# Kernel optimization log

Hardware: AMD Instinct MI355X
Metric: run time of the kernel (lower is better)

The kernel has to match this reference:

```python
import jax, jax.numpy as jnp
import numpy as np

H = 8        # num_heads
D = 768      # d_model
DH = D // H  # d_head = 96


def setup_inputs() -> dict:
    key = jax.random.key(0)
    ks = jax.random.split(key, 12)
    B, S = 4, 2048
    s_in = 1.0 / np.sqrt(D)
    s_cat = 1.0 / np.sqrt(D)
    return {
        "input_querys": jax.random.normal(ks[0], (B, S, D), jnp.float32),
        "input_key": jax.random.normal(ks[1], (B, S, D), jnp.float32),
        "input_values": jax.random.normal(ks[2], (B, S, D), jnp.float32),
        # per-head projection weights, stacked over the head axis
        "Wq": jax.random.normal(ks[3], (H, D, DH), jnp.float32) * s_in,
        "bq": jax.random.normal(ks[4], (H, DH), jnp.float32) * s_in,
        "Wk": jax.random.normal(ks[5], (H, D, DH), jnp.float32) * s_in,
        "bk": jax.random.normal(ks[6], (H, DH), jnp.float32) * s_in,
        "Wv": jax.random.normal(ks[7], (H, D, DH), jnp.float32) * s_in,
        "bv": jax.random.normal(ks[8], (H, DH), jnp.float32) * s_in,
        # output linear: (H*DH) -> D
        "Wo": jax.random.normal(ks[9], (H * DH, D), jnp.float32) * s_cat,
        "bo": jax.random.normal(ks[10], (D,), jnp.float32) * s_cat,
    }


def reference(input_querys, input_key, input_values, Wq, bq, Wk, bk, Wv, bv, Wo, bo):
    # Per-head linear projections (vectorized over the head axis)
    # q/k/v: [B,S,D] -> [B,H,S,DH]
    Q = jnp.einsum("bsd,hdk->bhsk", input_querys, Wq) + bq[None, :, None, :]
    K = jnp.einsum("bsd,hdk->bhsk", input_key, Wk) + bk[None, :, None, :]
    V = jnp.einsum("bsd,hdk->bhsk", input_values, Wv) + bv[None, :, None, :]

    scale = 1.0 / jnp.sqrt(jnp.asarray(DH, Q.dtype))
    scores = jnp.einsum("bhsk,bhtk->bhst", Q, K) * scale  # [B,H,S,S]
    attn = jax.nn.softmax(scores, axis=-1)
    out = jnp.einsum("bhst,bhtk->bhsk", attn, V)  # [B,H,S,DH]

    # concat heads (head-major order matches torch.cat over ModuleList)
    B, _, S, _ = out.shape
    cat = out.transpose(0, 2, 1, 3).reshape(B, S, H * DH)
    return cat @ Wo + bo
```

## Files before the change

kernel.cpp:

```cpp
#include <hip/hip_runtime.h>


typedef unsigned short u16;
typedef _Float16 h16;
typedef h16 h16x8 __attribute__((ext_vector_type(8)));
typedef __fp16 fp16x2 __attribute__((ext_vector_type(2)));
typedef unsigned short u16x8 __attribute__((ext_vector_type(8)));
typedef unsigned short u16x4 __attribute__((ext_vector_type(4)));
typedef float f32x4 __attribute__((ext_vector_type(4)));

__device__ __forceinline__ u16 f2h(float f) {
  union { h16 h; u16 u; } c; c.h = (h16)f; return c.u;
}

__device__ __forceinline__ void gll16(const void* g, void* l) {
  __builtin_amdgcn_global_load_lds(
      (const __attribute__((address_space(1))) void*)g,
      (__attribute__((address_space(3))) void*)l, 16, 0, 0);
}

__global__ __launch_bounds__(256) void prep_kernel(
    const float* __restrict__ Wq, const float* __restrict__ Wk,
    const float* __restrict__ Wv, const float* __restrict__ Wo,
    u16* __restrict__ WqT, u16* __restrict__ WkT,
    u16* __restrict__ WvT, u16* __restrict__ WoT)
{
  int idx = (blockIdx.x * 256 + threadIdx.x) * 8;
  int region = idx / 589824;
  int i = idx % 589824;
  int n = i / 768;
  int d = i % 768;
  u16x8 v;
  if (region == 3) {
    #pragma unroll
    for (int j = 0; j < 8; j++) v[j] = f2h(Wo[(size_t)(d + j) * 768 + n]);
    *(u16x8*)(&WoT[i]) = v;
  } else {
    int h = n / 96, kk = n % 96;
    const float* W = (region == 0) ? Wq : (region == 1) ? Wk : Wv;
    u16* T = (region == 0) ? WqT : (region == 1) ? WkT : WvT;
    #pragma unroll
    for (int j = 0; j < 8; j++) v[j] = f2h(W[(size_t)h * 73728 + (size_t)(d + j) * 96 + kk]);
    *(u16x8*)(&T[i]) = v;
  }
}

#define GK 768

__global__ __launch_bounds__(256) void gemm_qkv(
    const float* __restrict__ Xq, const float* __restrict__ Xk,
    const float* __restrict__ Xv, const u16* __restrict__ WT,
    const float* __restrict__ bq, const float* __restrict__ bk,
    const float* __restrict__ bv,
    u16* __restrict__ Q16, u16* __restrict__ K16, u16* __restrict__ VT)
{
  const int z = blockIdx.z;
  const float* A = (z == 0) ? Xq : (z == 1) ? Xk : Xv;
  const u16* BT = WT + (size_t)z * 589824;
  const float* bias = (z == 0) ? bq : (z == 1) ? bk : bv;

  __shared__ __align__(16) u16 As[128 * 32];
  __shared__ __align__(16) u16 Bs[64 * 32];
  const int tid = threadIdx.x;
  const int wave = tid >> 6;
  const int lane = tid & 63;
  const int quad = lane >> 4;
  const int l16 = lane & 15;
  const int m0 = blockIdx.x * 128;
  const int n0 = blockIdx.y * 64;

  f32x4 acc[2][4];
  #pragma unroll
  for (int i = 0; i < 2; i++)
    #pragma unroll
    for (int j = 0; j < 4; j++) acc[i][j] = (f32x4){0.f, 0.f, 0.f, 0.f};

  const int ar = tid >> 2;
  const int ac = (tid & 3) * 8;

  f32x4 pf[4];
  u16x8 pb;
  {
    pf[0] = *(const f32x4*)(&A[(size_t)(m0 + ar) * GK + ac]);
    pf[1] = *(const f32x4*)(&A[(size_t)(m0 + ar) * GK + ac + 4]);
    pf[2] = *(const f32x4*)(&A[(size_t)(m0 + 64 + ar) * GK + ac]);
    pf[3] = *(const f32x4*)(&A[(size_t)(m0 + 64 + ar) * GK + ac + 4]);
    pb = *(const u16x8*)(&BT[(size_t)(n0 + ar) * GK + ac]);
  }

  for (int kt = 0; kt < 24; kt++) {
    u16x8 h0, h1;
    #pragma unroll
    for (int j = 0; j < 4; j++) {
      h0[j] = f2h(pf[0][j]); h0[4 + j] = f2h(pf[1][j]);
      h1[j] = f2h(pf[2][j]); h1[4 + j] = f2h(pf[3][j]);
    }
    *(u16x8*)(&As[ar * 32 + ac]) = h0;
    *(u16x8*)(&As[(64 + ar) * 32 + ac]) = h1;
    *(u16x8*)(&Bs[ar * 32 + ac]) = pb;
    __syncthreads();

    if (kt + 1 < 24) {
      const int k0 = (kt + 1) * 32;
      pf[0] = *(const f32x4*)(&A[(size_t)(m0 + ar) * GK + k0 + ac]);
      pf[1] = *(const f32x4*)(&A[(size_t)(m0 + ar) * GK + k0 + ac + 4]);
      pf[2] = *(const f32x4*)(&A[(size_t)(m0 + 64 + ar) * GK + k0 + ac]);
      pf[3] = *(const f32x4*)(&A[(size_t)(m0 + 64 + ar) * GK + k0 + ac + 4]);
      pb = *(const u16x8*)(&BT[(size_t)(n0 + ar) * GK + k0 + ac]);
    }

    h16x8 af[2], bf[4];
    #pragma unroll
    for (int mf = 0; mf < 2; mf++)
      af[mf] = *(const h16x8*)(&As[(wave * 32 + mf * 16 + l16) * 32 + quad * 8]);
    #pragma unroll
    for (int nf = 0; nf < 4; nf++)
      bf[nf] = *(const h16x8*)(&Bs[(nf * 16 + l16) * 32 + quad * 8]);
    #pragma unroll
    for (int mf = 0; mf < 2; mf++)
      #pragma unroll
      for (int nf = 0; nf < 4; nf++)
        acc[mf][nf] = __builtin_amdgcn_mfma_f32_16x16x32_f16(af[mf], bf[nf], acc[mf][nf], 0, 0, 0);

    if (kt + 1 < 24) __syncthreads();
  }

  u16* Yr = (z == 0) ? Q16 : K16;
  #pragma unroll
  for (int nf = 0; nf < 4; nf++) {
    const int n = n0 + nf * 16 + l16;
    const float bv2 = bias[n];
    #pragma unroll
    for (int mf = 0; mf < 2; mf++) {
      const int m = m0 + wave * 32 + mf * 16 + quad * 4;
      if (z == 2) {
        const int b = m >> 11, s = m & 2047;
        u16x4 pk;
        #pragma unroll
        for (int r = 0; r < 4; r++) pk[r] = f2h(acc[mf][nf][r] + bv2);
        *(u16x4*)(&VT[(size_t)b * 768 * 2048 + (size_t)n * 2048 + s]) = pk;
      } else {
        #pragma unroll
        for (int r = 0; r < 4; r++)
          Yr[(size_t)(m + r) * GK + n] = f2h(acc[mf][nf][r] + bv2);
      }
    }
  }
}

__global__ __launch_bounds__(256) void gemm_o(
    const u16* __restrict__ A, const u16* __restrict__ BT,
    const float* __restrict__ bias, float* __restrict__ Y)
{
  __shared__ __align__(16) u16 As[128 * 32];
  __shared__ __align__(16) u16 Bs[64 * 32];
  const int tid = threadIdx.x;
  const int wave = tid >> 6;
  const int lane = tid & 63;
  const int quad = lane >> 4;
  const int l16 = lane & 15;
  const int m0 = blockIdx.x * 128;
  const int n0 = blockIdx.y * 64;

  f32x4 acc[2][4];
  #pragma unroll
  for (int i = 0; i < 2; i++)
    #pragma unroll
    for (int j = 0; j < 4; j++) acc[i][j] = (f32x4){0.f, 0.f, 0.f, 0.f};

  const int Lr = lane >> 2, Lc = (lane & 3) * 8;
  const u16* gA0 = A + (size_t)(m0 + wave * 32 + Lr) * GK + Lc;
  const u16* gA1 = gA0 + (size_t)16 * GK;
  const u16* gB  = BT + (size_t)(n0 + wave * 16 + Lr) * GK + Lc;
  u16* lA0 = &As[(wave * 32) * 32];
  u16* lA1 = &As[(wave * 32 + 16) * 32];
  u16* lB  = &Bs[(wave * 16) * 32];

  for (int kt = 0; kt < 24; kt++) {
    gll16(gA0, lA0);
    gll16(gA1, lA1);
    gll16(gB, lB);
    gA0 += 32; gA1 += 32; gB += 32;
    __syncthreads();

    h16x8 af[2], bf[4];
    #pragma unroll
    for (int mf = 0; mf < 2; mf++)
      af[mf] = *(const h16x8*)(&As[(wave * 32 + mf * 16 + l16) * 32 + quad * 8]);
    #pragma unroll
    for (int nf = 0; nf < 4; nf++)
      bf[nf] = *(const h16x8*)(&Bs[(nf * 16 + l16) * 32 + quad * 8]);
    #pragma unroll
    for (int mf = 0; mf < 2; mf++)
      #pragma unroll
      for (int nf = 0; nf < 4; nf++)
        acc[mf][nf] = __builtin_amdgcn_mfma_f32_16x16x32_f16(af[mf], bf[nf], acc[mf][nf], 0, 0, 0);
    __syncthreads();
  }

  #pragma unroll
  for (int nf = 0; nf < 4; nf++) {
    const int n = n0 + nf * 16 + l16;
    const float bv = bias[n];
    #pragma unroll
    for (int mf = 0; mf < 2; mf++) {
      const int m = m0 + wave * 32 + mf * 16 + quad * 4;
      #pragma unroll
      for (int r = 0; r < 4; r++)
        Y[(size_t)(m + r) * GK + n] = acc[mf][nf][r] + bv;
    }
  }
}

#define SEQ 2048
#define LQK 104
#define LVT 72
#define LPS 72

__global__ __launch_bounds__(512, 4) void attn_kernel(
    const u16* __restrict__ Q, const u16* __restrict__ K,
    const u16* __restrict__ VT, u16* __restrict__ O)
{
  __shared__ __align__(16) u16 Ks[64 * LQK];
  __shared__ __align__(16) u16 Vt[96 * LVT];
  __shared__ __align__(16) u16 Ps[8][16 * LPS];

  const int tid = threadIdx.x;
  const int wave = tid >> 6;
  const int lane = tid & 63;
  const int quad = lane >> 4;
  const int l16 = lane & 15;

  const int bh = blockIdx.y;
  const int b = bh >> 3, h = bh & 7;
  const int q0 = blockIdx.x * 128;

  const size_t batch_off = (size_t)b * SEQ * 768;
  const u16* Kg = K + batch_off + h * 96;
  const u16* Vg = VT + (size_t)b * 768 * 2048 + (size_t)(h * 96) * 2048;

  h16x8 qf[3];
  {
    const u16* Qrow = Q + batch_off + (size_t)(q0 + wave * 16 + l16) * 768 + h * 96 + quad * 8;
    #pragma unroll
    for (int ks = 0; ks < 3; ks++) qf[ks] = *(const h16x8*)(&Qrow[ks * 32]);
  }

  const int kr0 = tid / 12, kc0 = (tid % 12) * 8;
  const int kr1 = (tid + 512) / 12, kc1 = ((tid + 512) % 12) * 8;
  const int vr0 = tid >> 3, vc0 = (tid & 7) * 8;
  const int vr1 = (tid + 512) >> 3, vc1 = ((tid + 512) & 7) * 8;
  const bool extra = tid < 256;

  f32x4 o[6];
  #pragma unroll
  for (int i = 0; i < 6; i++) o[i] = (f32x4){0.f, 0.f, 0.f, 0.f};
  float m_raw = -1e30f, lrow = 0.f;
  const float sc = 0.14724498f;

  u16* Pw = &Ps[wave][0];

  u16x8 kA, kB, vA, vB;
  kA = *(const u16x8*)(&Kg[(size_t)kr0 * 768 + kc0]);
  vA = *(const u16x8*)(&Vg[(size_t)vr0 * 2048 + vc0]);
  if (extra) {
    kB = *(const u16x8*)(&Kg[(size_t)kr1 * 768 + kc1]);
    vB = *(const u16x8*)(&Vg[(size_t)vr1 * 2048 + vc1]);
  }

  for (int kt = 0; kt < SEQ / 64; kt++) {
    *(u16x8*)(&Ks[kr0 * LQK + kc0]) = kA;
    *(u16x8*)(&Vt[vr0 * LVT + vc0]) = vA;
    if (extra) {
      *(u16x8*)(&Ks[kr1 * LQK + kc1]) = kB;
      *(u16x8*)(&Vt[vr1 * LVT + vc1]) = vB;
    }
    __syncthreads();

    if (kt + 1 < SEQ / 64) {
      const u16* Kn = Kg + (size_t)(kt + 1) * 64 * 768;
      const u16* Vn = Vg + (size_t)(kt + 1) * 64;
      kA = *(const u16x8*)(&Kn[(size_t)kr0 * 768 + kc0]);
      vA = *(const u16x8*)(&Vn[(size_t)vr0 * 2048 + vc0]);
      if (extra) {
        kB = *(const u16x8*)(&Kn[(size_t)kr1 * 768 + kc1]);
        vB = *(const u16x8*)(&Vn[(size_t)vr1 * 2048 + vc1]);
      }
    }

    f32x4 s[4];
    #pragma unroll
    for (int kf = 0; kf < 4; kf++) s[kf] = (f32x4){0.f, 0.f, 0.f, 0.f};
    #pragma unroll
    for (int ks = 0; ks < 3; ks++) {
      #pragma unroll
      for (int kf = 0; kf < 4; kf++) {
        h16x8 a = *(const h16x8*)(&Ks[(kf * 16 + l16) * LQK + ks * 32 + quad * 8]);
        s[kf] = __builtin_amdgcn_mfma_f32_16x16x32_f16(a, qf[ks], s[kf], 0, 0, 0);
      }
    }

    float mx = s[0][0];
    #pragma unroll
    for (int kf = 0; kf < 4; kf++)
      #pragma unroll
      for (int r = 0; r < 4; r++) mx = fmaxf(mx, s[kf][r]);
    mx = fmaxf(mx, __shfl_xor(mx, 16));
    mx = fmaxf(mx, __shfl_xor(mx, 32));
    const float mold = m_raw;
    m_raw = fmaxf(mold, mx);
    const float c0 = sc * m_raw;
    float ps = 0.f;
    #pragma unroll
    for (int kf = 0; kf < 4; kf++)
      #pragma unroll
      for (int r = 0; r < 4; r++) {
        float p = exp2f(fmaf(s[kf][r], sc, -c0));
        s[kf][r] = p;
        ps += p;
      }
    if (__any(m_raw > mold)) {
      const float alpha = exp2f(sc * (mold - m_raw));
      lrow *= alpha;
      #pragma unroll
      for (int nfo = 0; nfo < 6; nfo++)
        #pragma unroll
        for (int r = 0; r < 4; r++) o[nfo][r] *= alpha;
    }
    lrow += ps;

    #pragma unroll
    for (int kf = 0; kf < 4; kf++)
      #pragma unroll
      for (int rp = 0; rp < 4; rp += 2) {
        fp16x2 pk = __builtin_amdgcn_cvt_pkrtz(s[kf][rp], s[kf][rp + 1]);
        *(fp16x2*)(&Pw[l16 * LPS + kf * 16 + quad * 4 + rp]) = pk;
      }

    #pragma unroll
    for (int ks = 0; ks < 2; ks++) {
      h16x8 pfr = *(const h16x8*)(&Pw[l16 * LPS + ks * 32 + quad * 8]);
      #pragma unroll
      for (int nfo = 0; nfo < 6; nfo++) {
        h16x8 vfr = *(const h16x8*)(&Vt[(nfo * 16 + l16) * LVT + ks * 32 + quad * 8]);
        o[nfo] = __builtin_amdgcn_mfma_f32_16x16x32_f16(vfr, pfr, o[nfo], 0, 0, 0);
      }
    }
    __syncthreads();
  }

  lrow += __shfl_xor(lrow, 16);
  lrow += __shfl_xor(lrow, 32);
  const float inv = 1.0f / lrow;
  u16* Ob = O + batch_off + (size_t)(q0 + wave * 16 + l16) * 768 + h * 96;
  #pragma unroll
  for (int nfo = 0; nfo < 6; nfo++) {
    fp16x2 lo = __builtin_amdgcn_cvt_pkrtz(o[nfo][0] * inv, o[nfo][1] * inv);
    fp16x2 hi = __builtin_amdgcn_cvt_pkrtz(o[nfo][2] * inv, o[nfo][3] * inv);
    *(fp16x2*)(&Ob[nfo * 16 + quad * 4]) = lo;
    *(fp16x2*)(&Ob[nfo * 16 + quad * 4 + 2]) = hi;
  }
}

extern "C" void kernel_launch(void* const* d_in, const int* in_sizes, int n_in,
                              void* d_out, int out_size, void* d_ws, size_t ws_size,
                              hipStream_t stream) {
  const float* Xq = (const float*)d_in[0];
  const float* Xk = (const float*)d_in[1];
  const float* Xv = (const float*)d_in[2];
  const float* Wq = (const float*)d_in[3];
  const float* bq = (const float*)d_in[4];
  const float* Wk = (const float*)d_in[5];
  const float* bk = (const float*)d_in[6];
  const float* Wv = (const float*)d_in[7];
  const float* bv = (const float*)d_in[8];
  const float* Wo = (const float*)d_in[9];
  const float* bo = (const float*)d_in[10];

  u16* wsu = (u16*)d_ws;
  u16* WT  = wsu;
  u16* WoT = wsu + 3 * 589824;
  u16* Q16 = wsu + 4 * 589824;

  u16* outu = (u16*)d_out;
  u16* VTb = outu;
  u16* K16 = outu + 6291456;

  u16* A16 = (u16*)d_in[0];

  prep_kernel<<<1152, 256, 0, stream>>>(Wq, Wk, Wv, Wo, WT, WT + 589824, WT + 2 * 589824, WoT);
  gemm_qkv<<<dim3(64, 12, 3), 256, 0, stream>>>(Xq, Xk, Xv, WT, bq, bk, bv, Q16, K16, VTb);
  attn_kernel<<<dim3(16, 32), 512, 0, stream>>>(Q16, K16, VTb, A16);
  gemm_o<<<dim3(64, 12), 256, 0, stream>>>(A16, WoT, bo, (float*)d_out);
}
```

Baseline: 312.0 us.

## Give each attention wave two query tiles and swap GEMM grid axes

The attention kernel now runs 256-thread blocks where each wave handles 32 query rows as two 16-row sets. Each K and V fragment read from LDS then feeds two MFMAs, which halves LDS fragment traffic per unit of compute. Per-thread register use roughly doubles for accumulators and Q fragments, and launch bounds drop to 256 threads with 3 blocks per SM. Separately, both GEMM launches swap grid x/y so consecutive blocks walk along N and share the same A rows, which should improve cache locality.

After: 355.9 us. +14.1%, slower.

```diff
diff --git a/kernel.cpp b/kernel.cpp
--- a/kernel.cpp
+++ b/kernel.cpp
@@ -66,8 +66,8 @@
   const int lane = tid & 63;
   const int quad = lane >> 4;
   const int l16 = lane & 15;
-  const int m0 = blockIdx.x * 128;
-  const int n0 = blockIdx.y * 64;
+  const int m0 = blockIdx.y * 128;
+  const int n0 = blockIdx.x * 64;
 
   f32x4 acc[2][4];
   #pragma unroll
@@ -159,8 +159,8 @@
   const int lane = tid & 63;
   const int quad = lane >> 4;
   const int l16 = lane & 15;
-  const int m0 = blockIdx.x * 128;
-  const int n0 = blockIdx.y * 64;
+  const int m0 = blockIdx.y * 128;
+  const int n0 = blockIdx.x * 64;
 
   f32x4 acc[2][4];
   #pragma unroll
@@ -217,13 +217,13 @@
 #define LVT 72
 #define LPS 72
 
-__global__ __launch_bounds__(512, 4) void attn_kernel(
+__global__ __launch_bounds__(256, 3) void attn_kernel(
     const u16* __restrict__ Q, const u16* __restrict__ K,
     const u16* __restrict__ VT, u16* __restrict__ O)
 {
   __shared__ __align__(16) u16 Ks[64 * LQK];
   __shared__ __align__(16) u16 Vt[96 * LVT];
-  __shared__ __align__(16) u16 Ps[8][16 * LPS];
+  __shared__ __align__(16) u16 Ps[4][32 * LPS];
 
   const int tid = threadIdx.x;
   const int wave = tid >> 6;
@@ -239,126 +239,140 @@
   const u16* Kg = K + batch_off + h * 96;
   const u16* Vg = VT + (size_t)b * 768 * 2048 + (size_t)(h * 96) * 2048;
 
-  h16x8 qf[3];
-  {
-    const u16* Qrow = Q + batch_off + (size_t)(q0 + wave * 16 + l16) * 768 + h * 96 + quad * 8;
-    #pragma unroll
-    for (int ks = 0; ks < 3; ks++) qf[ks] = *(const h16x8*)(&Qrow[ks * 32]);
-  }
-
-  const int kr0 = tid / 12, kc0 = (tid % 12) * 8;
-  const int kr1 = (tid + 512) / 12, kc1 = ((tid + 512) % 12) * 8;
-  const int vr0 = tid >> 3, vc0 = (tid & 7) * 8;
-  const int vr1 = (tid + 512) >> 3, vc1 = ((tid + 512) & 7) * 8;
-  const bool extra = tid < 256;
-
-  f32x4 o[6];
-  #pragma unroll
-  for (int i = 0; i < 6; i++) o[i] = (f32x4){0.f, 0.f, 0.f, 0.f};
-  float m_raw = -1e30f, lrow = 0.f;
+  h16x8 qf[2][3];
+  #pragma unroll
+  for (int set = 0; set < 2; set++) {
+    const u16* Qrow = Q + batch_off + (size_t)(q0 + wave * 32 + set * 16 + l16) * 768 + h * 96 + quad * 8;
+    #pragma unroll
+    for (int ks = 0; ks < 3; ks++) qf[set][ks] = *(const h16x8*)(&Qrow[ks * 32]);
+  }
+
+  int krr[3], kcc[3], vrr[3], vcc[3];
+  #pragma unroll
+  for (int j = 0; j < 3; j++) {
+    int c = tid + j * 256;
+    krr[j] = c / 12;  kcc[j] = (c % 12) * 8;
+    vrr[j] = c >> 3;  vcc[j] = (c & 7) * 8;
+  }
+
+  f32x4 o[2][6];
+  #pragma unroll
+  for (int set = 0; set < 2; set++)
+    #pragma unroll
+    for (int i = 0; i < 6; i++) o[set][i] = (f32x4){0.f, 0.f, 0.f, 0.f};
+  float m_raw[2] = {-1e30f, -1e30f}, lrow[2] = {0.f, 0.f};
   const float sc = 0.14724498f;
 
   u16* Pw = &Ps[wave][0];
 
-  u16x8 kA, kB, vA, vB;
-  kA = *(const u16x8*)(&Kg[(size_t)kr0 * 768 + kc0]);
-  vA = *(const u16x8*)(&Vg[(size_t)vr0 * 2048 + vc0]);
-  if (extra) {
-    kB = *(const u16x8*)(&Kg[(size_t)kr1 * 768 + kc1]);
-    vB = *(const u16x8*)(&Vg[(size_t)vr1 * 2048 + vc1]);
+  u16x8 kA[3], vA[3];
+  #pragma unroll
+  for (int j = 0; j < 3; j++) {
+    kA[j] = *(const u16x8*)(&Kg[(size_t)krr[j] * 768 + kcc[j]]);
+    vA[j] = *(const u16x8*)(&Vg[(size_t)vrr[j] * 2048 + vcc[j]]);
   }
 
   for (int kt = 0; kt < SEQ / 64; kt++) {
-    *(u16x8*)(&Ks[kr0 * LQK + kc0]) = kA;
-    *(u16x8*)(&Vt[vr0 * LVT + vc0]) = vA;
-    if (extra) {
-      *(u16x8*)(&Ks[kr1 * LQK + kc1]) = kB;
-      *(u16x8*)(&Vt[vr1 * LVT + vc1]) = vB;
+    #pragma unroll
+    for (int j = 0; j < 3; j++) {
+      *(u16x8*)(&Ks[krr[j] * LQK + kcc[j]]) = kA[j];
+      *(u16x8*)(&Vt[vrr[j] * LVT + vcc[j]]) = vA[j];
     }
     __syncthreads();
 
     if (kt + 1 < SEQ / 64) {
       const u16* Kn = Kg + (size_t)(kt + 1) * 64 * 768;
       const u16* Vn = Vg + (size_t)(kt + 1) * 64;
-      kA = *(const u16x8*)(&Kn[(size_t)kr0 * 768 + kc0]);
-      vA = *(const u16x8*)(&Vn[(size_t)vr0 * 2048 + vc0]);
-      if (extra) {
-        kB = *(const u16x8*)(&Kn[(size_t)kr1 * 768 + kc1]);
-        vB = *(const u16x8*)(&Vn[(size_t)vr1 * 2048 + vc1]);
+      #pragma unroll
+      for (int j = 0; j < 3; j++) {
+        kA[j] = *(const u16x8*)(&Kn[(size_t)krr[j] * 768 + kcc[j]]);
+        vA[j] = *(const u16x8*)(&Vn[(size_t)vrr[j] * 2048 + vcc[j]]);
       }
     }
 
-    f32x4 s[4];
-    #pragma unroll
-    for (int kf = 0; kf < 4; kf++) s[kf] = (f32x4){0.f, 0.f, 0.f, 0.f};
+    f32x4 s[2][4];
+    #pragma unroll
+    for (int set = 0; set < 2; set++)
+      #pragma unroll
+      for (int kf = 0; kf < 4; kf++) s[set][kf] = (f32x4){0.f, 0.f, 0.f, 0.f};
     #pragma unroll
     for (int ks = 0; ks < 3; ks++) {
       #pragma unroll
       for (int kf = 0; kf < 4; kf++) {
         h16x8 a = *(const h16x8*)(&Ks[(kf * 16 + l16) * LQK + ks * 32 + quad * 8]);
-        s[kf] = __builtin_amdgcn_mfma_f32_16x16x32_f16(a, qf[ks], s[kf], 0, 0, 0);
+        s[0][kf] = __builtin_amdgcn_mfma_f32_16x16x32_f16(a, qf[0][ks], s[0][kf], 0, 0, 0);
+        s[1][kf] = __builtin_amdgcn_mfma_f32_16x16x32_f16(a, qf[1][ks], s[1][kf], 0, 0, 0);
       }
     }
 
-    float mx = s[0][0];
-    #pragma unroll
-    for (int kf = 0; kf < 4; kf++)
-      #pragma unroll
-      for (int r = 0; r < 4; r++) mx = fmaxf(mx, s[kf][r]);
-    mx = fmaxf(mx, __shfl_xor(mx, 16));
-    mx = fmaxf(mx, __shfl_xor(mx, 32));
-    const float mold = m_raw;
-    m_raw = fmaxf(mold, mx);
-    const float c0 = sc * m_raw;
-    float ps = 0.f;
-    #pragma unroll
-    for (int kf = 0; kf < 4; kf++)
-      #pragma unroll
-      for (int r = 0; r < 4; r++) {
-        float p = exp2f(fmaf(s[kf][r], sc, -c0));
-        s[kf][r] = p;
-        ps += p;
+    #pragma unroll
+    for (int set = 0; set < 2; set++) {
+      float mx = s[set][0][0];
+      #pragma unroll
+      for (int kf = 0; kf < 4; kf++)
+        #pragma unroll
+        for (int r = 0; r < 4; r++) mx = fmaxf(mx, s[set][kf][r]);
+      mx = fmaxf(mx, __shfl_xor(mx, 16));
+      mx = fmaxf(mx, __shfl_xor(mx, 32));
+      const float mold = m_raw[set];
+      m_raw[set] = fmaxf(mold, mx);
+      const float c0 = sc * m_raw[set];
+      float ps = 0.f;
+      #pragma unroll
+      for (int kf = 0; kf < 4; kf++)
+        #pragma unroll
+        for (int r = 0; r < 4; r++) {
+          float p = exp2f(fmaf(s[set][kf][r], sc, -c0));
+          s[set][kf][r] = p;
+          ps += p;
+        }
+      if (__any(m_raw[set] > mold)) {
+        const float alpha = exp2f(sc * (mold - m_raw[set]));
+        lrow[set] *= alpha;
+        #pragma unroll
+        for (int nfo = 0; nfo < 6; nfo++)
+          #pragma unroll
+          for (int r = 0; r < 4; r++) o[set][nfo][r] *= alpha;
       }
-    if (__any(m_raw > mold)) {
-      const float alpha = exp2f(sc * (mold - m_raw));
-      lrow *= alpha;
-      #pragma unroll
-      for (int nfo = 0; nfo < 6; nfo++)
-        #pragma unroll
-        for (int r = 0; r < 4; r++) o[nfo][r] *= alpha;
-    }
-    lrow += ps;
-
-    #pragma unroll
-    for (int kf = 0; kf < 4; kf++)
-      #pragma unroll
-      for (int rp = 0; rp < 4; rp += 2) {
-        fp16x2 pk = __builtin_amdgcn_cvt_pkrtz(s[kf][rp], s[kf][rp + 1]);
-        *(fp16x2*)(&Pw[l16 * LPS + kf * 16 + quad * 4 + rp]) = pk;
-      }
+      lrow[set] += ps;
+
+      #pragma unroll
+      for (int kf = 0; kf < 4; kf++)
+        #pragma unroll
+        for (int rp = 0; rp < 4; rp += 2) {
+          fp16x2 pk = __builtin_amdgcn_cvt_pkrtz(s[set][kf][rp], s[set][kf][rp + 1]);
+          *(fp16x2*)(&Pw[(set * 16 + l16) * LPS + kf * 16 + quad * 4 + rp]) = pk;
+        }
+    }
 
     #pragma unroll
     for (int ks = 0; ks < 2; ks++) {
-      h16x8 pfr = *(const h16x8*)(&Pw[l16 * LPS + ks * 32 + quad * 8]);
+      h16x8 p0 = *(const h16x8*)(&Pw[l16 * LPS + ks * 32 + quad * 8]);
+      h16x8 p1 = *(const h16x8*)(&Pw[(16 + l16) * LPS + ks * 32 + quad * 8]);
       #pragma unroll
       for (int nfo = 0; nfo < 6; nfo++) {
         h16x8 vfr = *(const h16x8*)(&Vt[(nfo * 16 + l16) * LVT + ks * 32 + quad * 8]);
-        o[nfo] = __builtin_amdgcn_mfma_f32_16x16x32_f16(vfr, pfr, o[nfo], 0, 0, 0);
+        o[0][nfo] = __builtin_amdgcn_mfma_f32_16x16x32_f16(vfr, p0, o[0][nfo], 0, 0, 0);
+        o[1][nfo] = __builtin_amdgcn_mfma_f32_16x16x32_f16(vfr, p1, o[1][nfo], 0, 0, 0);
       }
     }
     __syncthreads();
   }
 
-  lrow += __shfl_xor(lrow, 16);
-  lrow += __shfl_xor(lrow, 32);
-  const float inv = 1.0f / lrow;
-  u16* Ob = O + batch_off + (size_t)(q0 + wave * 16 + l16) * 768 + h * 96;
-  #pragma unroll
-  for (int nfo = 0; nfo < 6; nfo++) {
-    fp16x2 lo = __builtin_amdgcn_cvt_pkrtz(o[nfo][0] * inv, o[nfo][1] * inv);
-    fp16x2 hi = __builtin_amdgcn_cvt_pkrtz(o[nfo][2] * inv, o[nfo][3] * inv);
-    *(fp16x2*)(&Ob[nfo * 16 + quad * 4]) = lo;
-    *(fp16x2*)(&Ob[nfo * 16 + quad * 4 + 2]) = hi;
+  #pragma unroll
+  for (int set = 0; set < 2; set++) {
+    float l = lrow[set];
+    l += __shfl_xor(l, 16);
+    l += __shfl_xor(l, 32);
+    const float inv = 1.0f / l;
+    u16* Ob = O + batch_off + (size_t)(q0 + wave * 32 + set * 16 + l16) * 768 + h * 96;
+    #pragma unroll
+    for (int nfo = 0; nfo < 6; nfo++) {
+      fp16x2 lo = __builtin_amdgcn_cvt_pkrtz(o[set][nfo][0] * inv, o[set][nfo][1] * inv);
+      fp16x2 hi = __builtin_amdgcn_cvt_pkrtz(o[set][nfo][2] * inv, o[set][nfo][3] * inv);
+      *(fp16x2*)(&Ob[nfo * 16 + quad * 4]) = lo;
+      *(fp16x2*)(&Ob[nfo * 16 + quad * 4 + 2]) = hi;
+    }
   }
 }
 
@@ -389,7 +403,7 @@
   u16* A16 = (u16*)d_in[0];
 
   prep_kernel<<<1152, 256, 0, stream>>>(Wq, Wk, Wv, Wo, WT, WT + 589824, WT + 2 * 589824, WoT);
-  gemm_qkv<<<dim3(64, 12, 3), 256, 0, stream>>>(Xq, Xk, Xv, WT, bq, bk, bv, Q16, K16, VTb);
-  attn_kernel<<<dim3(16, 32), 512, 0, stream>>>(Q16, K16, VTb, A16);
-  gemm_o<<<dim3(64, 12), 256, 0, stream>>>(A16, WoT, bo, (float*)d_out);
-}
+  gemm_qkv<<<dim3(12, 64, 3), 256, 0, stream>>>(Xq, Xk, Xv, WT, bq, bk, bv, Q16, K16, VTb);
+  attn_kernel<<<dim3(16, 32), 256, 0, stream>>>(Q16, K16, VTb, A16);
+  gemm_o<<<dim3(12, 64), 256, 0, stream>>>(A16, WoT, bo, (float*)d_out);
+}
```
